# Optimization experiments

Hardware: AMD Instinct MI355X
Metric: run time of the kernel (lower is better)

The kernel has to match this reference:

```python
import jax, jax.numpy as jnp
import numpy as np

N_EMBED = 1024
N_HEAD = 16
EPS = 1.1920929e-07  # torch.finfo(float32).eps, nn.RMSNorm default eps=None


def rmsnorm(x, w):
    var = jnp.mean(x * x, axis=-1, keepdims=True)
    return x * jax.lax.rsqrt(var + EPS) * w


def setup_inputs() -> dict:
    key = jax.random.key(0)
    ks = jax.random.split(key, 12)
    d = N_EMBED
    s = lambda fan_in: 1.0 / np.sqrt(fan_in)
    inp = {
        "x": jax.random.normal(ks[0], (2, 2048, d), jnp.float32),
        "w_attn": jax.random.uniform(ks[1], (d, 3 * d), jnp.float32, -s(d), s(d)),
        "b_attn": jax.random.uniform(ks[2], (3 * d,), jnp.float32, -s(d), s(d)),
        "w_proj": jax.random.uniform(ks[3], (d, d), jnp.float32, -s(d), s(d)),
        "b_proj": jax.random.uniform(ks[4], (d,), jnp.float32, -s(d), s(d)),
        "w_fc1": jax.random.uniform(ks[5], (d, 4 * d), jnp.float32, -s(d), s(d)),
        "b_fc1": jax.random.uniform(ks[6], (4 * d,), jnp.float32, -s(d), s(d)),
        "w_fc2": jax.random.uniform(ks[7], (4 * d, d), jnp.float32, -s(4 * d), s(4 * d)),
        "b_fc2": jax.random.uniform(ks[8], (d,), jnp.float32, -s(4 * d), s(4 * d)),
        "g_norm1": jnp.ones((d,), jnp.float32),
        "g_norm2": jnp.ones((d,), jnp.float32),
    }
    return inp


def reference(x, w_attn, b_attn, w_proj, b_proj, w_fc1, b_fc1, w_fc2, b_fc2, g_norm1, g_norm2):
    B, T, d = x.shape
    H = N_HEAD
    hd = d // H

    # --- attention branch ---
    h = rmsnorm(x, g_norm1)
    qkv = h @ w_attn + b_attn  # [B,T,3d]
    q, k, v = jnp.split(qkv, 3, axis=-1)
    q = q.reshape(B, T, H, hd).transpose(0, 2, 1, 3)  # [B,H,T,hd]
    k = k.reshape(B, T, H, hd).transpose(0, 2, 1, 3)
    v = v.reshape(B, T, H, hd).transpose(0, 2, 1, 3)
    qk = jnp.einsum('bhqd,bhkd->bhqk', q, k)  # NOTE: no logit scaling (as in source)
    mask = jnp.tril(jnp.ones((T, T), bool))
    qk = jnp.where(mask, qk, -jnp.inf)
    # source scales softmax OUTPUT by n_embed**-0.5 (faithful quirk)
    attn = jax.nn.softmax(qk, axis=-1) * (d ** -0.5)
    o = jnp.einsum('bhqk,bhkd->bhqd', attn, v)
    o = o.transpose(0, 2, 1, 3).reshape(B, T, d)
    x = x + (o @ w_proj + b_proj)

    # --- MLP branch ---
    h = rmsnorm(x, g_norm2)
    h = jax.nn.gelu(h @ w_fc1 + b_fc1, approximate=False)
    x = x + (h @ w_fc2 + b_fc2)
    return x
```

## Files before the change

### kernel.cpp

```cpp
#include <hip/hip_runtime.h>
#include <hip/hip_bf16.h>


typedef __hip_bfloat16 bf16;
typedef __attribute__((ext_vector_type(8))) short short8;
typedef __attribute__((ext_vector_type(4))) float floatx4;

__device__ __forceinline__ float bits2f(unsigned short u) {
  union { unsigned int i; float f; } c; c.i = ((unsigned int)u) << 16; return c.f;
}
__device__ __forceinline__ unsigned short f2bits(float f) {
  bf16 b = __float2bfloat16(f);
  union { bf16 b; unsigned short u; } c; c.b = b; return c.u;
}

__device__ __forceinline__ void gld_lds16(const unsigned short* g, unsigned short* l) {
  __builtin_amdgcn_global_load_lds(
      (const __attribute__((address_space(1))) void*)g,
      (__attribute__((address_space(3))) void*)l, 16, 0, 0);
}

__global__ __launch_bounds__(256) void rmsnorm_r15(const float* __restrict__ x,
                                                   const float* __restrict__ g,
                                                   unsigned short* __restrict__ out)
{
  const int row = blockIdx.x, tid = threadIdx.x;
  const size_t rb = (size_t)row * 1024;
  float4 xv = *(const float4*)(x + rb + tid * 4);
  float v[4] = {xv.x, xv.y, xv.z, xv.w};
  float s = v[0]*v[0] + v[1]*v[1] + v[2]*v[2] + v[3]*v[3];
  #pragma unroll
  for (int off = 32; off > 0; off >>= 1) s += __shfl_down(s, off, 64);
  __shared__ float part[4];
  if ((tid & 63) == 0) part[tid >> 6] = s;
  __syncthreads();
  const float tot = part[0] + part[1] + part[2] + part[3];
  const float sc = rsqrtf(tot * (1.0f / 1024.0f) + 1.1920929e-07f);
  float4 gv = *(const float4*)(g + tid * 4);
  ushort4 o4 = { f2bits(v[0] * sc * gv.x), f2bits(v[1] * sc * gv.y),
                 f2bits(v[2] * sc * gv.z), f2bits(v[3] * sc * gv.w) };
  *(ushort4*)(out + rb + tid * 4) = o4;
}

__global__ __launch_bounds__(256) void wprep_r15(const float* __restrict__ in,
                                                 unsigned short* __restrict__ out,
                                                 int K, int N)
{
  __shared__ unsigned short tile[32][33];
  const int tid = threadIdx.x;
  const int k0 = blockIdx.y * 32, n0 = blockIdx.x * 32;
  const int tr = tid >> 3, tc4 = (tid & 7) * 4;
  float4 v = *(const float4*)(in + (size_t)(k0 + tr) * N + n0 + tc4);
  tile[tr][tc4 + 0] = f2bits(v.x);
  tile[tr][tc4 + 1] = f2bits(v.y);
  tile[tr][tc4 + 2] = f2bits(v.z);
  tile[tr][tc4 + 3] = f2bits(v.w);
  __syncthreads();
  ushort4 o = { tile[tc4 + 0][tr], tile[tc4 + 1][tr],
                tile[tc4 + 2][tr], tile[tc4 + 3][tr] };
  *(ushort4*)(out + (size_t)(n0 + tr) * K + k0 + tc4) = o;
}

template<int EPI>
__global__ __launch_bounds__(256) void gemm128_r15(
    const unsigned short* __restrict__ A,
    const unsigned short* __restrict__ BT,
    const float* __restrict__ bias,
    const float* __restrict__ resid,
    void* __restrict__ Cout,
    int M, int N, int K, int Klen)
{
  __shared__ __align__(16) unsigned short As[2][128 * 32];
  __shared__ __align__(16) unsigned short Bs[2][128 * 32];
  const int tid = threadIdx.x;
  const int lane = tid & 63;
  const int wv = tid >> 6;
  const int m0 = blockIdx.y * 128, n0 = blockIdx.x * 128;
  const int wm = (wv >> 1) * 64, wn = (wv & 1) * 64;
  const int kbase = blockIdx.z * Klen;

  const int s0 = tid, s1 = tid + 256;
  const int r0 = s0 >> 2, kq0 = (s0 & 3) ^ ((r0 >> 1) & 3);
  const int r1 = s1 >> 2, kq1 = (s1 & 3) ^ ((r1 >> 1) & 3);
  const unsigned short* Ab = A  + (size_t)m0 * K;
  const unsigned short* Bb = BT + (size_t)n0 * K;
  const size_t ga0 = (size_t)r0 * K + kq0 * 8 + kbase;
  const size_t ga1 = (size_t)r1 * K + kq1 * 8 + kbase;

  floatx4 acc[4][4];
  #pragma unroll
  for (int i = 0; i < 4; ++i)
    #pragma unroll
    for (int j = 0; j < 4; ++j)
      acc[i][j] = (floatx4){0.f, 0.f, 0.f, 0.f};

  int aoff[4], boff[4];
  #pragma unroll
  for (int i = 0; i < 4; ++i) {
    int ra = wm + i * 16 + (lane & 15);
    aoff[i] = (ra * 4 + ((lane >> 4) ^ ((ra >> 1) & 3))) * 8;
    int rb = wn + i * 16 + (lane & 15);
    boff[i] = (rb * 4 + ((lane >> 4) ^ ((rb >> 1) & 3))) * 8;
  }

  gld_lds16(Ab + ga0, As[0] + s0 * 8);
  gld_lds16(Ab + ga1, As[0] + s1 * 8);
  gld_lds16(Bb + ga0, Bs[0] + s0 * 8);
  gld_lds16(Bb + ga1, Bs[0] + s1 * 8);
  __syncthreads();

  const int nsteps = Klen >> 5;
  for (int t = 0; t < nsteps; ++t) {
    const int cur = t & 1;
    if (t + 1 < nsteps) {
      const size_t ko = (size_t)(t + 1) * 32;
      gld_lds16(Ab + ga0 + ko, As[cur ^ 1] + s0 * 8);
      gld_lds16(Ab + ga1 + ko, As[cur ^ 1] + s1 * 8);
      gld_lds16(Bb + ga0 + ko, Bs[cur ^ 1] + s0 * 8);
      gld_lds16(Bb + ga1 + ko, Bs[cur ^ 1] + s1 * 8);
    }

    short8 af[4], bfr[4];
    #pragma unroll
    for (int i = 0; i < 4; ++i) {
      af[i]  = *(const short8*)(As[cur] + aoff[i]);
      bfr[i] = *(const short8*)(Bs[cur] + boff[i]);
    }
    #pragma unroll
    for (int i = 0; i < 4; ++i)
      #pragma unroll
      for (int j = 0; j < 4; ++j)
        acc[i][j] = __builtin_amdgcn_mfma_f32_16x16x32_bf16(af[i], bfr[j], acc[i][j], 0, 0, 0);

    __syncthreads();
  }

  float* Cp32 = (float*)Cout;
  if constexpr (EPI == 4) Cp32 += (size_t)blockIdx.z * ((size_t)M * N);

  #pragma unroll
  for (int i = 0; i < 4; ++i) {
    #pragma unroll
    for (int j = 0; j < 4; ++j) {
      const int rbase = m0 + wm + i * 16 + (lane >> 4) * 4;
      const int c = n0 + wn + j * 16 + (lane & 15);
      float bia = 0.0f;
      if constexpr (EPI != 4) bia = bias[c];
      #pragma unroll
      for (int r = 0; r < 4; ++r) {
        float v = acc[i][j][r] + bia;
        const size_t idx = (size_t)(rbase + r) * N + c;
        if constexpr (EPI == 0) {
          ((unsigned short*)Cout)[idx] = f2bits(v);
        } else if constexpr (EPI == 1) {
          ((float*)Cout)[idx] = v + resid[idx];
        } else if constexpr (EPI == 2) {
          v = 0.5f * v * (1.0f + erff(v * 0.70710678118654752f));
          ((unsigned short*)Cout)[idx] = f2bits(v);
        } else if constexpr (EPI == 3) {
          ((float*)Cout)[idx] = v + resid[idx];
        } else {
          Cp32[idx] = v;
        }
      }
    }
  }
}

template<int EPI>
__global__ __launch_bounds__(512) void gemm256_r15(
    const unsigned short* __restrict__ A,
    const unsigned short* __restrict__ BT,
    const float* __restrict__ bias,
    void* __restrict__ Cout,
    int M, int N, int K)
{
  __shared__ __align__(16) unsigned short As[4][256 * 32];
  __shared__ __align__(16) unsigned short Bs[4][256 * 32];
  const int tid = threadIdx.x;
  const int lane = tid & 63, wv = tid >> 6;
  const int quad = lane >> 4, l15 = lane & 15;
  const int m0 = blockIdx.y * 256, n0 = blockIdx.x * 256;
  const int wm = (wv >> 2) * 128, wn = (wv & 3) * 64;

  const int s0 = tid, s1 = tid + 512;
  const int r0 = s0 >> 2, kq0 = (s0 & 3) ^ ((r0 >> 1) & 3);
  const int r1 = s1 >> 2, kq1 = (s1 & 3) ^ ((r1 >> 1) & 3);
  const unsigned short* Ab = A  + (size_t)m0 * K;
  const unsigned short* Bb = BT + (size_t)n0 * K;
  const size_t ga0 = (size_t)r0 * K + kq0 * 8;
  const size_t ga1 = (size_t)r1 * K + kq1 * 8;

  floatx4 acc[8][4];
  #pragma unroll
  for (int i = 0; i < 8; ++i)
    #pragma unroll
    for (int j = 0; j < 4; ++j)
      acc[i][j] = (floatx4){0.f, 0.f, 0.f, 0.f};

  int aoff[8], boff[4];
  #pragma unroll
  for (int i = 0; i < 8; ++i) {
    int ra = wm + i * 16 + l15;
    aoff[i] = (ra * 4 + (quad ^ ((ra >> 1) & 3))) * 8;
  }
  #pragma unroll
  for (int j = 0; j < 4; ++j) {
    int rb = wn + j * 16 + l15;
    boff[j] = (rb * 4 + (quad ^ ((rb >> 1) & 3))) * 8;
  }

  #define STG_R15(t) { const size_t ko = (size_t)(t) * 32; const int bb = (t) & 3; \
    gld_lds16(Ab + ga0 + ko, As[bb] + s0 * 8); \
    gld_lds16(Ab + ga1 + ko, As[bb] + s1 * 8); \
    gld_lds16(Bb + ga0 + ko, Bs[bb] + s0 * 8); \
    gld_lds16(Bb + ga1 + ko, Bs[bb] + s1 * 8); }

  STG_R15(0);
  STG_R15(1);

  const int nsteps = K >> 5;
  for (int t = 0; t < nsteps; ++t) {
    const int cur = t & 3;
    if (t + 2 < nsteps) {
      STG_R15(t + 2);
      asm volatile("s_waitcnt vmcnt(8)" ::: "memory");
    } else if (t + 1 < nsteps) {
      asm volatile("s_waitcnt vmcnt(4)" ::: "memory");
    } else {
      asm volatile("s_waitcnt vmcnt(0)" ::: "memory");
    }
    __builtin_amdgcn_s_barrier();
    asm volatile("" ::: "memory");

    short8 bfr[4];
    #pragma unroll
    for (int j = 0; j < 4; ++j)
      bfr[j] = *(const short8*)(Bs[cur] + boff[j]);
    #pragma unroll
    for (int ih = 0; ih < 2; ++ih) {
      short8 af[4];
      #pragma unroll
      for (int k = 0; k < 4; ++k)
        af[k] = *(const short8*)(As[cur] + aoff[ih * 4 + k]);
      #pragma unroll
      for (int k = 0; k < 4; ++k)
        #pragma unroll
        for (int j = 0; j < 4; ++j)
          acc[ih * 4 + k][j] = __builtin_amdgcn_mfma_f32_16x16x32_bf16(af[k], bfr[j], acc[ih * 4 + k][j], 0, 0, 0);
    }
  }
  #undef STG_R15

  #pragma unroll
  for (int i = 0; i < 8; ++i) {
    #pragma unroll
    for (int j = 0; j < 4; ++j) {
      const int rbase = m0 + wm + i * 16 + quad * 4;
      const int c = n0 + wn + j * 16 + l15;
      const float bia = bias[c];
      #pragma unroll
      for (int r = 0; r < 4; ++r) {
        float v = acc[i][j][r] + bia;
        const size_t idx = (size_t)(rbase + r) * N + c;
        if constexpr (EPI == 2) {
          v = 0.5f * v * (1.0f + erff(v * 0.70710678118654752f));
        }
        ((unsigned short*)Cout)[idx] = f2bits(v);
      }
    }
  }
}

__global__ __launch_bounds__(256) void red2_r15(const float* __restrict__ P,
                                                const float* __restrict__ resid,
                                                const float* __restrict__ bias,
                                                float* __restrict__ out)
{
  const size_t i = ((size_t)blockIdx.x * 256 + threadIdx.x) * 4;
  const int col = (int)(i & 1023);
  float4 p0 = *(const float4*)(P + i);
  float4 p1 = *(const float4*)(P + ((size_t)4096 * 1024) + i);
  float4 xr = *(const float4*)(resid + i);
  float4 b  = *(const float4*)(bias + col);
  float4 o  = { p0.x + p1.x + xr.x + b.x, p0.y + p1.y + xr.y + b.y,
                p0.z + p1.z + xr.z + b.z, p0.w + p1.w + xr.w + b.w };
  *(float4*)(out + i) = o;
}

__global__ __launch_bounds__(512) void attn_r15(const unsigned short* __restrict__ qkv,
                                                unsigned short* __restrict__ o)
{
  __shared__ __align__(16) unsigned short Qs[128 * 64];
  __shared__ __align__(16) unsigned short Ks[2][64 * 64];
  __shared__ __align__(16) unsigned short VT[2][64 * 72];
  __shared__ __align__(16) unsigned short Ps[128 * 72];
  __shared__ __align__(16) float stat_s[128];

  const int tid = threadIdx.x, lane = tid & 63, wv = tid >> 6;
  const int quad = lane >> 4, l15 = lane & 15;
  const int qt0 = blockIdx.x, bh = blockIdx.y;
  const int b = bh >> 4, h = bh & 15;
  const size_t base = (size_t)b * 2048 * 3072;
  const int qcol = h * 64, kcol = 1024 + h * 64, vcol = 2048 + h * 64;

  const int sr = tid >> 3, scp = tid & 7, sc = scp ^ (sr & 7);
  const unsigned short* kgp = qkv + base + (size_t)sr * 3072 + kcol + sc * 8;
  const int vp = tid & 31, vdc = tid >> 5;
  const unsigned short* vgp = qkv + base + (size_t)(2 * vp) * 3072 + vcol + vdc * 4;

  for (int pass = 0; pass < 2; ++pass) {
    const int qt = pass ? qt0 : 15 - qt0;
    const int q0 = qt * 128;
    const int nkt = 2 * qt + 2;

    __syncthreads();

    #pragma unroll
    for (int p = 0; p < 2; ++p) {
      int s = tid + 512 * p;
      int r = s >> 3, cp = s & 7, c = cp ^ (r & 7);
      gld_lds16(qkv + base + (size_t)(q0 + r) * 3072 + qcol + c * 8, Qs + s * 8);
    }
    gld_lds16(kgp, Ks[0] + tid * 8);
    {
      uint2 u0 = *(const uint2*)vgp;
      uint2 u1 = *(const uint2*)(vgp + 3072);
      unsigned short* dst = VT[0] + (size_t)(vdc * 4) * 72 + 2 * vp;
      *(unsigned int*)(dst + 0 * 72) = (u0.x & 0xffffu) | (u1.x << 16);
      *(unsigned int*)(dst + 1 * 72) = (u0.x >> 16)     | (u1.x & 0xffff0000u);
      *(unsigned int*)(dst + 2 * 72) = (u0.y & 0xffffu) | (u1.y << 16);
      *(unsigned int*)(dst + 3 * 72) = (u0.y >> 16)     | (u1.y & 0xffff0000u);
    }
    __syncthreads();

    short8 qa[2];
    #pragma unroll
    for (int ks = 0; ks < 2; ++ks) {
      int ra = wv * 16 + l15;
      int cp = (ks * 4 + quad) ^ (ra & 7);
      qa[ks] = *(const short8*)(Qs + (ra * 8 + cp) * 8);
    }

    floatx4 oacc[4];
    #pragma unroll
    for (int dt = 0; dt < 4; ++dt) oacc[dt] = (floatx4){0.f, 0.f, 0.f, 0.f};
    float m_i[4], l_i[4];
    #pragma unroll
    for (int r = 0; r < 4; ++r) { m_i[r] = -3.0e38f; l_i[r] = 0.0f; }

    for (int kt = 0; kt < nkt; ++kt) {
      const int cur = kt & 1;
      const bool pf = (kt + 1 < nkt);
      uint2 u0, u1;
      if (pf) {
        const size_t koff = (size_t)(kt + 1) * 64 * 3072;
        gld_lds16(kgp + koff, Ks[cur ^ 1] + tid * 8);
        u0 = *(const uint2*)(vgp + koff);
        u1 = *(const uint2*)(vgp + koff + 3072);
      }

      short8 kb[4][2];
      #pragma unroll
      for (int j = 0; j < 4; ++j)
        #pragma unroll
        for (int ks = 0; ks < 2; ++ks) {
          int rb = j * 16 + l15;
          int cp = (ks * 4 + quad) ^ (rb & 7);
          kb[j][ks] = *(const short8*)(Ks[cur] + (rb * 8 + cp) * 8);
        }
      floatx4 s_[4];
      #pragma unroll
      for (int j = 0; j < 4; ++j) s_[j] = (floatx4){0.f, 0.f, 0.f, 0.f};
      #pragma unroll
      for (int j = 0; j < 4; ++j)
        #pragma unroll
        for (int ks = 0; ks < 2; ++ks)
          s_[j] = __builtin_amdgcn_mfma_f32_16x16x32_bf16(qa[ks], kb[j][ks], s_[j], 0, 0, 0);

      const int k0 = kt * 64;
      const int rowmin = q0 + wv * 16;
      const int rowb = rowmin + quad * 4;
      if (k0 + 63 > rowmin) {
        #pragma unroll
        for (int j = 0; j < 4; ++j) {
          const int col = k0 + j * 16 + l15;
          #pragma unroll
          for (int r = 0; r < 4; ++r)
            if (col > rowb + r) s_[j][r] = -3.0e38f;
        }
      }
      float fm[4], al[4], rs[4];
      #pragma unroll
      for (int r = 0; r < 4; ++r)
        fm[r] = fmaxf(fmaxf(s_[0][r], s_[1][r]), fmaxf(s_[2][r], s_[3][r]));
      #pragma unroll
      for (int msk = 1; msk < 16; msk <<= 1)
        #pragma unroll
        for (int r = 0; r < 4; ++r)
          fm[r] = fmaxf(fm[r], __shfl_xor(fm[r], msk, 64));
      #pragma unroll
      for (int r = 0; r < 4; ++r) {
        const float mn = fmaxf(m_i[r], fm[r]);
        al[r] = __expf(m_i[r] - mn);
        m_i[r] = mn;
      }
      #pragma unroll
      for (int j = 0; j < 4; ++j)
        #pragma unroll
        for (int r = 0; r < 4; ++r)
          s_[j][r] = __expf(s_[j][r] - m_i[r]);
      #pragma unroll
      for (int r = 0; r < 4; ++r)
        rs[r] = (s_[0][r] + s_[1][r]) + (s_[2][r] + s_[3][r]);
      #pragma unroll
      for (int msk = 1; msk < 16; msk <<= 1)
        #pragma unroll
        for (int r = 0; r < 4; ++r)
          rs[r] += __shfl_xor(rs[r], msk, 64);
      #pragma unroll
      for (int r = 0; r < 4; ++r)
        l_i[r] = l_i[r] * al[r] + rs[r];
      if (l15 == 0) {
        float4 a4 = { al[0], al[1], al[2], al[3] };
        *(float4*)(stat_s + wv * 16 + quad * 4) = a4;
      }
      #pragma unroll
      for (int j = 0; j < 4; ++j)
        #pragma unroll
        for (int r = 0; r < 4; ++r)
          Ps[(size_t)(wv * 16 + quad * 4 + r) * 72 + j * 16 + l15] = f2bits(s_[j][r]);

      const float alq = stat_s[wv * 16 + l15];
      #pragma unroll
      for (int dt = 0; dt < 4; ++dt)
        #pragma unroll
        for (int r = 0; r < 4; ++r)
          oacc[dt][r] *= alq;

      short8 va[4][2], pb[2];
      #pragma unroll
      for (int dt = 0; dt < 4; ++dt)
        #pragma unroll
        for (int ks = 0; ks < 2; ++ks)
          va[dt][ks] = *(const short8*)(VT[cur] + (size_t)(dt * 16 + l15) * 72 + ks * 32 + quad * 8);
      #pragma unroll
      for (int ks = 0; ks < 2; ++ks)
        pb[ks] = *(const short8*)(Ps + (size_t)(wv * 16 + l15) * 72 + ks * 32 + quad * 8);
      #pragma unroll
      for (int dt = 0; dt < 4; ++dt)
        #pragma unroll
        for (int ks = 0; ks < 2; ++ks)
          oacc[dt] = __builtin_amdgcn_mfma_f32_16x16x32_bf16(va[dt][ks], pb[ks], oacc[dt], 0, 0, 0);

      if (pf) {
        unsigned short* dst = VT[cur ^ 1] + (size_t)(vdc * 4) * 72 + 2 * vp;
        *(unsigned int*)(dst + 0 * 72) = (u0.x & 0xffffu) | (u1.x << 16);
        *(unsigned int*)(dst + 1 * 72) = (u0.x >> 16)     | (u1.x & 0xffff0000u);
        *(unsigned int*)(dst + 2 * 72) = (u0.y & 0xffffu) | (u1.y << 16);
        *(unsigned int*)(dst + 3 * 72) = (u0.y >> 16)     | (u1.y & 0xffff0000u);
      }
      __syncthreads();
    }

    if (l15 == 0) {
      float4 l4 = { l_i[0], l_i[1], l_i[2], l_i[3] };
      *(float4*)(stat_s + wv * 16 + quad * 4) = l4;
    }
    const float linv = 0.03125f / stat_s[wv * 16 + l15];
    const size_t row = (size_t)b * 2048 + q0 + wv * 16 + l15;
    #pragma unroll
    for (int dt = 0; dt < 4; ++dt) {
      const int col = h * 64 + dt * 16 + quad * 4;
      ushort4 o4 = { f2bits(oacc[dt][0] * linv), f2bits(oacc[dt][1] * linv),
                     f2bits(oacc[dt][2] * linv), f2bits(oacc[dt][3] * linv) };
      *(ushort4*)(o + row * 1024 + col) = o4;
    }
  }
}

extern "C" void kernel_launch(void* const* d_in, const int* in_sizes, int n_in,
                              void* d_out, int out_size, void* d_ws, size_t ws_size,
                              hipStream_t stream)
{
  (void)in_sizes; (void)n_in; (void)out_size; (void)ws_size;
  const float* x      = (const float*)d_in[0];
  const float* w_attn = (const float*)d_in[1];
  const float* b_attn = (const float*)d_in[2];
  const float* w_proj = (const float*)d_in[3];
  const float* b_proj = (const float*)d_in[4];
  const float* w_fc1  = (const float*)d_in[5];
  const float* b_fc1  = (const float*)d_in[6];
  const float* w_fc2  = (const float*)d_in[7];
  const float* b_fc2  = (const float*)d_in[8];
  const float* g1     = (const float*)d_in[9];
  const float* g2     = (const float*)d_in[10];
  float* out = (float*)d_out;

  char* ws = (char*)d_ws;
  unsigned short* h   = (unsigned short*)(ws);
  unsigned short* qkv = (unsigned short*)(ws + ((size_t)8  << 20));
  unsigned short* ov  = (unsigned short*)(ws);
  float*          x1  = (float*)         (ws + ((size_t)32 << 20));
  unsigned short* h2  = (unsigned short*)(ws + ((size_t)8  << 20));
  unsigned short* h3  = (unsigned short*)(ws + ((size_t)48 << 20));
  unsigned short* WT  = (unsigned short*)(ws + ((size_t)80 << 20));
  float*          P   = (float*)(ws);

  const int M = 4096;

  rmsnorm_r15<<<M, 256, 0, stream>>>(x, g1, h);
  wprep_r15<<<dim3(3072 / 32, 1024 / 32), 256, 0, stream>>>(w_attn, WT, 1024, 3072);
  gemm256_r15<0><<<dim3(3072 / 256, M / 256), 512, 0, stream>>>(h, WT, b_attn, qkv, M, 3072, 1024);
  attn_r15<<<dim3(8, 32), 512, 0, stream>>>(qkv, ov);
  wprep_r15<<<dim3(1024 / 32, 1024 / 32), 256, 0, stream>>>(w_proj, WT, 1024, 1024);
  gemm128_r15<1><<<dim3(1024 / 128, M / 128), 256, 0, stream>>>(ov, WT, b_proj, x, x1, M, 1024, 1024, 1024);
  rmsnorm_r15<<<M, 256, 0, stream>>>(x1, g2, h2);
  wprep_r15<<<dim3(4096 / 32, 1024 / 32), 256, 0, stream>>>(w_fc1, WT, 1024, 4096);
  gemm256_r15<2><<<dim3(4096 / 256, M / 256), 512, 0, stream>>>(h2, WT, b_fc1, h3, M, 4096, 1024);
  wprep_r15<<<dim3(1024 / 32, 4096 / 32), 256, 0, stream>>>(w_fc2, WT, 4096, 1024);
  gemm128_r15<4><<<dim3(1024 / 128, M / 128, 2), 256, 0, stream>>>(h3, WT, nullptr, nullptr, P, M, 1024, 4096, 2048);
  red2_r15<<<4096, 256, 0, stream>>>(P, x1, b_fc2, out);
}
```

Baseline: 379.4 us.

## Deepen attention K/V prefetch to two tiles ahead with triple-buffered K

The attention kernel's key/value loop now prefetches two tiles ahead instead of one. K is triple-buffered in LDS, and V values are ping-ponged through two register sets via a manually unrolled-by-two loop. Full __syncthreads are replaced with explicit vmcnt/lgkmcnt waits plus s_barrier, to hide global load latency behind the MFMA and softmax work. The cost is extra LDS (one more K tile) and extra registers, which may reduce occupancy. Hand-tuned waitcnt values risk correctness if the instruction ordering changes.

```diff
diff --git a/kernel.cpp b/kernel.cpp
--- a/kernel.cpp
+++ b/kernel.cpp
@@ -20,7 +20,7 @@
       (__attribute__((address_space(3))) void*)l, 16, 0, 0);
 }
 
-__global__ __launch_bounds__(256) void rmsnorm_r15(const float* __restrict__ x,
+__global__ __launch_bounds__(256) void rmsnorm_r17(const float* __restrict__ x,
                                                    const float* __restrict__ g,
                                                    unsigned short* __restrict__ out)
 {
@@ -42,7 +42,7 @@
   *(ushort4*)(out + rb + tid * 4) = o4;
 }
 
-__global__ __launch_bounds__(256) void wprep_r15(const float* __restrict__ in,
+__global__ __launch_bounds__(256) void wprep_r17(const float* __restrict__ in,
                                                  unsigned short* __restrict__ out,
                                                  int K, int N)
 {
@@ -62,7 +62,7 @@
 }
 
 template<int EPI>
-__global__ __launch_bounds__(256) void gemm128_r15(
+__global__ __launch_bounds__(256) void gemm128_r17(
     const unsigned short* __restrict__ A,
     const unsigned short* __restrict__ BT,
     const float* __restrict__ bias,
@@ -168,7 +168,7 @@
 }
 
 template<int EPI>
-__global__ __launch_bounds__(512) void gemm256_r15(
+__global__ __launch_bounds__(512) void gemm256_r17(
     const unsigned short* __restrict__ A,
     const unsigned short* __restrict__ BT,
     const float* __restrict__ bias,
@@ -210,20 +210,20 @@
     boff[j] = (rb * 4 + (quad ^ ((rb >> 1) & 3))) * 8;
   }
 
-  #define STG_R15(t) { const size_t ko = (size_t)(t) * 32; const int bb = (t) & 3; \
+  #define STG_R17(t) { const size_t ko = (size_t)(t) * 32; const int bb = (t) & 3; \
     gld_lds16(Ab + ga0 + ko, As[bb] + s0 * 8); \
     gld_lds16(Ab + ga1 + ko, As[bb] + s1 * 8); \
     gld_lds16(Bb + ga0 + ko, Bs[bb] + s0 * 8); \
     gld_lds16(Bb + ga1 + ko, Bs[bb] + s1 * 8); }
 
-  STG_R15(0);
-  STG_R15(1);
+  STG_R17(0);
+  STG_R17(1);
 
   const int nsteps = K >> 5;
   for (int t = 0; t < nsteps; ++t) {
     const int cur = t & 3;
     if (t + 2 < nsteps) {
-      STG_R15(t + 2);
+      STG_R17(t + 2);
       asm volatile("s_waitcnt vmcnt(8)" ::: "memory");
     } else if (t + 1 < nsteps) {
       asm volatile("s_waitcnt vmcnt(4)" ::: "memory");
@@ -250,7 +250,7 @@
           acc[ih * 4 + k][j] = __builtin_amdgcn_mfma_f32_16x16x32_bf16(af[k], bfr[j], acc[ih * 4 + k][j], 0, 0, 0);
     }
   }
-  #undef STG_R15
+  #undef STG_R17
 
   #pragma unroll
   for (int i = 0; i < 8; ++i) {
@@ -272,7 +272,7 @@
   }
 }
 
-__global__ __launch_bounds__(256) void red2_r15(const float* __restrict__ P,
+__global__ __launch_bounds__(256) void red2_r17(const float* __restrict__ P,
                                                 const float* __restrict__ resid,
                                                 const float* __restrict__ bias,
                                                 float* __restrict__ out)
@@ -288,11 +288,11 @@
   *(float4*)(out + i) = o;
 }
 
-__global__ __launch_bounds__(512) void attn_r15(const unsigned short* __restrict__ qkv,
+__global__ __launch_bounds__(512) void attn_r17(const unsigned short* __restrict__ qkv,
                                                 unsigned short* __restrict__ o)
 {
   __shared__ __align__(16) unsigned short Qs[128 * 64];
-  __shared__ __align__(16) unsigned short Ks[2][64 * 64];
+  __shared__ __align__(16) unsigned short Ks[3][64 * 64];
   __shared__ __align__(16) unsigned short VT[2][64 * 72];
   __shared__ __align__(16) unsigned short Ps[128 * 72];
   __shared__ __align__(16) float stat_s[128];
@@ -308,6 +308,8 @@
   const unsigned short* kgp = qkv + base + (size_t)sr * 3072 + kcol + sc * 8;
   const int vp = tid & 31, vdc = tid >> 5;
   const unsigned short* vgp = qkv + base + (size_t)(2 * vp) * 3072 + vcol + vdc * 4;
+  unsigned short* KsB = &Ks[0][0];
+  const int t8 = tid * 8;
 
   for (int pass = 0; pass < 2; ++pass) {
     const int qt = pass ? qt0 : 15 - qt0;
@@ -322,17 +324,25 @@
       int r = s >> 3, cp = s & 7, c = cp ^ (r & 7);
       gld_lds16(qkv + base + (size_t)(q0 + r) * 3072 + qcol + c * 8, Qs + s * 8);
     }
-    gld_lds16(kgp, Ks[0] + tid * 8);
+    gld_lds16(kgp, KsB + t8);
+    uint2 vA0, vA1, vB0, vB1;
+    if (nkt > 1) gld_lds16(kgp + (size_t)64 * 3072, KsB + 4096 + t8);
+    vA0 = *(const uint2*)vgp;
+    vA1 = *(const uint2*)(vgp + 3072);
+    if (nkt > 1) {
+      vB0 = *(const uint2*)(vgp + (size_t)64 * 3072);
+      vB1 = *(const uint2*)(vgp + (size_t)64 * 3072 + 3072);
+    }
+    asm volatile("s_waitcnt vmcnt(2)" ::: "memory");
     {
-      uint2 u0 = *(const uint2*)vgp;
-      uint2 u1 = *(const uint2*)(vgp + 3072);
       unsigned short* dst = VT[0] + (size_t)(vdc * 4) * 72 + 2 * vp;
-      *(unsigned int*)(dst + 0 * 72) = (u0.x & 0xffffu) | (u1.x << 16);
-      *(unsigned int*)(dst + 1 * 72) = (u0.x >> 16)     | (u1.x & 0xffff0000u);
-      *(unsigned int*)(dst + 2 * 72) = (u0.y & 0xffffu) | (u1.y << 16);
-      *(unsigned int*)(dst + 3 * 72) = (u0.y >> 16)     | (u1.y & 0xffff0000u);
-    }
-    __syncthreads();
+      *(unsigned int*)(dst + 0 * 72) = (vA0.x & 0xffffu) | (vA1.x << 16);
+      *(unsigned int*)(dst + 1 * 72) = (vA0.x >> 16)     | (vA1.x & 0xffff0000u);
+      *(unsigned int*)(dst + 2 * 72) = (vA0.y & 0xffffu) | (vA1.y << 16);
+      *(unsigned int*)(dst + 3 * 72) = (vA0.y >> 16)     | (vA1.y & 0xffff0000u);
+    }
+    asm volatile("s_waitcnt lgkmcnt(0)" ::: "memory");
+    __builtin_amdgcn_s_barrier();
 
     short8 qa[2];
     #pragma unroll
@@ -349,119 +359,126 @@
     #pragma unroll
     for (int r = 0; r < 4; ++r) { m_i[r] = -3.0e38f; l_i[r] = 0.0f; }
 
-    for (int kt = 0; kt < nkt; ++kt) {
-      const int cur = kt & 1;
-      const bool pf = (kt + 1 < nkt);
-      uint2 u0, u1;
-      if (pf) {
-        const size_t koff = (size_t)(kt + 1) * 64 * 3072;
-        gld_lds16(kgp + koff, Ks[cur ^ 1] + tid * 8);
-        u0 = *(const uint2*)(vgp + koff);
-        u1 = *(const uint2*)(vgp + koff + 3072);
-      }
-
-      short8 kb[4][2];
-      #pragma unroll
-      for (int j = 0; j < 4; ++j)
-        #pragma unroll
-        for (int ks = 0; ks < 2; ++ks) {
-          int rb = j * 16 + l15;
-          int cp = (ks * 4 + quad) ^ (rb & 7);
-          kb[j][ks] = *(const short8*)(Ks[cur] + (rb * 8 + cp) * 8);
-        }
-      floatx4 s_[4];
-      #pragma unroll
-      for (int j = 0; j < 4; ++j) s_[j] = (floatx4){0.f, 0.f, 0.f, 0.f};
-      #pragma unroll
-      for (int j = 0; j < 4; ++j)
-        #pragma unroll
-        for (int ks = 0; ks < 2; ++ks)
-          s_[j] = __builtin_amdgcn_mfma_f32_16x16x32_bf16(qa[ks], kb[j][ks], s_[j], 0, 0, 0);
-
-      const int k0 = kt * 64;
-      const int rowmin = q0 + wv * 16;
-      const int rowb = rowmin + quad * 4;
-      if (k0 + 63 > rowmin) {
-        #pragma unroll
-        for (int j = 0; j < 4; ++j) {
-          const int col = k0 + j * 16 + l15;
-          #pragma unroll
-          for (int r = 0; r < 4; ++r)
-            if (col > rowb + r) s_[j][r] = -3.0e38f;
-        }
-      }
-      float fm[4], al[4], rs[4];
-      #pragma unroll
-      for (int r = 0; r < 4; ++r)
-        fm[r] = fmaxf(fmaxf(s_[0][r], s_[1][r]), fmaxf(s_[2][r], s_[3][r]));
-      #pragma unroll
-      for (int msk = 1; msk < 16; msk <<= 1)
-        #pragma unroll
-        for (int r = 0; r < 4; ++r)
-          fm[r] = fmaxf(fm[r], __shfl_xor(fm[r], msk, 64));
-      #pragma unroll
-      for (int r = 0; r < 4; ++r) {
-        const float mn = fmaxf(m_i[r], fm[r]);
-        al[r] = __expf(m_i[r] - mn);
-        m_i[r] = mn;
-      }
-      #pragma unroll
-      for (int j = 0; j < 4; ++j)
-        #pragma unroll
-        for (int r = 0; r < 4; ++r)
-          s_[j][r] = __expf(s_[j][r] - m_i[r]);
-      #pragma unroll
-      for (int r = 0; r < 4; ++r)
-        rs[r] = (s_[0][r] + s_[1][r]) + (s_[2][r] + s_[3][r]);
-      #pragma unroll
-      for (int msk = 1; msk < 16; msk <<= 1)
-        #pragma unroll
-        for (int r = 0; r < 4; ++r)
-          rs[r] += __shfl_xor(rs[r], msk, 64);
-      #pragma unroll
-      for (int r = 0; r < 4; ++r)
-        l_i[r] = l_i[r] * al[r] + rs[r];
-      if (l15 == 0) {
-        float4 a4 = { al[0], al[1], al[2], al[3] };
-        *(float4*)(stat_s + wv * 16 + quad * 4) = a4;
-      }
-      #pragma unroll
-      for (int j = 0; j < 4; ++j)
-        #pragma unroll
-        for (int r = 0; r < 4; ++r)
-          Ps[(size_t)(wv * 16 + quad * 4 + r) * 72 + j * 16 + l15] = f2bits(s_[j][r]);
-
-      const float alq = stat_s[wv * 16 + l15];
-      #pragma unroll
-      for (int dt = 0; dt < 4; ++dt)
-        #pragma unroll
-        for (int r = 0; r < 4; ++r)
-          oacc[dt][r] *= alq;
-
-      short8 va[4][2], pb[2];
-      #pragma unroll
-      for (int dt = 0; dt < 4; ++dt)
-        #pragma unroll
-        for (int ks = 0; ks < 2; ++ks)
-          va[dt][ks] = *(const short8*)(VT[cur] + (size_t)(dt * 16 + l15) * 72 + ks * 32 + quad * 8);
-      #pragma unroll
-      for (int ks = 0; ks < 2; ++ks)
-        pb[ks] = *(const short8*)(Ps + (size_t)(wv * 16 + l15) * 72 + ks * 32 + quad * 8);
-      #pragma unroll
-      for (int dt = 0; dt < 4; ++dt)
-        #pragma unroll
-        for (int ks = 0; ks < 2; ++ks)
-          oacc[dt] = __builtin_amdgcn_mfma_f32_16x16x32_bf16(va[dt][ks], pb[ks], oacc[dt], 0, 0, 0);
-
-      if (pf) {
-        unsigned short* dst = VT[cur ^ 1] + (size_t)(vdc * 4) * 72 + 2 * vp;
-        *(unsigned int*)(dst + 0 * 72) = (u0.x & 0xffffu) | (u1.x << 16);
-        *(unsigned int*)(dst + 1 * 72) = (u0.x >> 16)     | (u1.x & 0xffff0000u);
-        *(unsigned int*)(dst + 2 * 72) = (u0.y & 0xffffu) | (u1.y << 16);
-        *(unsigned int*)(dst + 3 * 72) = (u0.y >> 16)     | (u1.y & 0xffff0000u);
-      }
-      __syncthreads();
-    }
+#define AITER_R17(KT, LV0, LV1, WV0, WV1)                                        \
+    {                                                                            \
+      const int kt_ = (KT);                                                      \
+      const bool pf2_ = (kt_ + 2 < nkt);                                         \
+      const bool pf1_ = (kt_ + 1 < nkt);                                         \
+      if (pf2_) {                                                                \
+        const size_t koff_ = (size_t)(kt_ + 2) * 64 * 3072;                      \
+        gld_lds16(kgp + koff_, KsB + ((kt_ + 2) % 3) * 4096 + t8);               \
+        LV0 = *(const uint2*)(vgp + koff_);                                      \
+        LV1 = *(const uint2*)(vgp + koff_ + 3072);                               \
+      }                                                                          \
+      const unsigned short* Kcur_ = KsB + (kt_ % 3) * 4096;                      \
+      const unsigned short* Vcur_ = VT[kt_ & 1];                                 \
+      short8 kb[4][2];                                                           \
+      _Pragma("unroll")                                                          \
+      for (int j = 0; j < 4; ++j)                                                \
+        _Pragma("unroll")                                                        \
+        for (int ks = 0; ks < 2; ++ks) {                                         \
+          int rb = j * 16 + l15;                                                 \
+          int cp = (ks * 4 + quad) ^ (rb & 7);                                   \
+          kb[j][ks] = *(const short8*)(Kcur_ + (rb * 8 + cp) * 8);               \
+        }                                                                        \
+      floatx4 s_[4];                                                             \
+      _Pragma("unroll")                                                          \
+      for (int j = 0; j < 4; ++j) s_[j] = (floatx4){0.f, 0.f, 0.f, 0.f};         \
+      _Pragma("unroll")                                                          \
+      for (int j = 0; j < 4; ++j)                                                \
+        _Pragma("unroll")                                                        \
+        for (int ks = 0; ks < 2; ++ks)                                           \
+          s_[j] = __builtin_amdgcn_mfma_f32_16x16x32_bf16(qa[ks], kb[j][ks], s_[j], 0, 0, 0); \
+      const int k0_ = kt_ * 64;                                                  \
+      const int rowmin_ = q0 + wv * 16;                                          \
+      const int rowb_ = rowmin_ + quad * 4;                                      \
+      if (k0_ + 63 > rowmin_) {                                                  \
+        _Pragma("unroll")                                                        \
+        for (int j = 0; j < 4; ++j) {                                            \
+          const int col_ = k0_ + j * 16 + l15;                                   \
+          _Pragma("unroll")                                                      \
+          for (int r = 0; r < 4; ++r)                                            \
+            if (col_ > rowb_ + r) s_[j][r] = -3.0e38f;                           \
+        }                                                                        \
+      }                                                                          \
+      float fm[4], al[4], rs[4];                                                 \
+      _Pragma("unroll")                                                          \
+      for (int r = 0; r < 4; ++r)                                                \
+        fm[r] = fmaxf(fmaxf(s_[0][r], s_[1][r]), fmaxf(s_[2][r], s_[3][r]));     \
+      _Pragma("unroll")                                                          \
+      for (int msk = 1; msk < 16; msk <<= 1)                                     \
+        _Pragma("unroll")                                                        \
+        for (int r = 0; r < 4; ++r)                                              \
+          fm[r] = fmaxf(fm[r], __shfl_xor(fm[r], msk, 64));                      \
+      _Pragma("unroll")                                                          \
+      for (int r = 0; r < 4; ++r) {                                              \
+        const float mn = fmaxf(m_i[r], fm[r]);                                   \
+        al[r] = __expf(m_i[r] - mn);                                             \
+        m_i[r] = mn;                                                             \
+      }                                                                          \
+      _Pragma("unroll")                                                          \
+      for (int j = 0; j < 4; ++j)                                                \
+        _Pragma("unroll")                                                        \
+        for (int r = 0; r < 4; ++r)                                              \
+          s_[j][r] = __expf(s_[j][r] - m_i[r]);                                  \
+      _Pragma("unroll")                                                          \
+      for (int r = 0; r < 4; ++r)                                                \
+        rs[r] = (s_[0][r] + s_[1][r]) + (s_[2][r] + s_[3][r]);                   \
+      _Pragma("unroll")                                                          \
+      for (int msk = 1; msk < 16; msk <<= 1)                                     \
+        _Pragma("unroll")                                                        \
+        for (int r = 0; r < 4; ++r)                                              \
+          rs[r] += __shfl_xor(rs[r], msk, 64);                                   \
+      _Pragma("unroll")                                                          \
+      for (int r = 0; r < 4; ++r)                                                \
+        l_i[r] = l_i[r] * al[r] + rs[r];                                         \
+      if (l15 == 0) {                                                            \
+        float4 a4 = { al[0], al[1], al[2], al[3] };                              \
+        *(float4*)(stat_s + wv * 16 + quad * 4) = a4;                            \
+      }                                                                          \
+      _Pragma("unroll")                                                          \
+      for (int j = 0; j < 4; ++j)                                                \
+        _Pragma("unroll")                                                        \
+        for (int r = 0; r < 4; ++r)                                              \
+          Ps[(size_t)(wv * 16 + quad * 4 + r) * 72 + j * 16 + l15] = f2bits(s_[j][r]); \
+      const float alq_ = stat_s[wv * 16 + l15];                                  \
+      _Pragma("unroll")                                                          \
+      for (int dt = 0; dt < 4; ++dt)                                             \
+        _Pragma("unroll")                                                        \
+        for (int r = 0; r < 4; ++r)                                              \
+          oacc[dt][r] *= alq_;                                                   \
+      short8 va[4][2], pb[2];                                                    \
+      _Pragma("unroll")                                                          \
+      for (int dt = 0; dt < 4; ++dt)                                             \
+        _Pragma("unroll")                                                        \
+        for (int ks = 0; ks < 2; ++ks)                                           \
+          va[dt][ks] = *(const short8*)(Vcur_ + (size_t)(dt * 16 + l15) * 72 + ks * 32 + quad * 8); \
+      _Pragma("unroll")                                                          \
+      for (int ks = 0; ks < 2; ++ks)                                             \
+        pb[ks] = *(const short8*)(Ps + (size_t)(wv * 16 + l15) * 72 + ks * 32 + quad * 8); \
+      _Pragma("unroll")                                                          \
+      for (int dt = 0; dt < 4; ++dt)                                             \
+        _Pragma("unroll")                                                        \
+        for (int ks = 0; ks < 2; ++ks)                                           \
+          oacc[dt] = __builtin_amdgcn_mfma_f32_16x16x32_bf16(va[dt][ks], pb[ks], oacc[dt], 0, 0, 0); \
+      if (pf1_) {                                                                \
+        if (pf2_) { asm volatile("s_waitcnt vmcnt(3)" ::: "memory"); }           \
+        else      { asm volatile("s_waitcnt vmcnt(0)" ::: "memory"); }           \
+        unsigned short* dst = VT[(kt_ + 1) & 1] + (size_t)(vdc * 4) * 72 + 2 * vp; \
+        *(unsigned int*)(dst + 0 * 72) = (WV0.x & 0xffffu) | (WV1.x << 16);      \
+        *(unsigned int*)(dst + 1 * 72) = (WV0.x >> 16)     | (WV1.x & 0xffff0000u); \
+        *(unsigned int*)(dst + 2 * 72) = (WV0.y & 0xffffu) | (WV1.y << 16);      \
+        *(unsigned int*)(dst + 3 * 72) = (WV0.y >> 16)     | (WV1.y & 0xffff0000u); \
+      }                                                                          \
+      asm volatile("s_waitcnt lgkmcnt(0)" ::: "memory");                         \
+      __builtin_amdgcn_s_barrier();                                              \
+    }
+
+    for (int t = 0; t < nkt; t += 2) {
+      AITER_R17(t,     vA0, vA1, vB0, vB1);
+      AITER_R17(t + 1, vB0, vB1, vA0, vA1);
+    }
+#undef AITER_R17
 
     if (l15 == 0) {
       float4 l4 = { l_i[0], l_i[1], l_i[2], l_i[3] };
@@ -509,16 +526,16 @@
 
   const int M = 4096;
 
-  rmsnorm_r15<<<M, 256, 0, stream>>>(x, g1, h);
-  wprep_r15<<<dim3(3072 / 32, 1024 / 32), 256, 0, stream>>>(w_attn, WT, 1024, 3072);
-  gemm256_r15<0><<<dim3(3072 / 256, M / 256), 512, 0, stream>>>(h, WT, b_attn, qkv, M, 3072, 1024);
-  attn_r15<<<dim3(8, 32), 512, 0, stream>>>(qkv, ov);
-  wprep_r15<<<dim3(1024 / 32, 1024 / 32), 256, 0, stream>>>(w_proj, WT, 1024, 1024);
-  gemm128_r15<1><<<dim3(1024 / 128, M / 128), 256, 0, stream>>>(ov, WT, b_proj, x, x1, M, 1024, 1024, 1024);
-  rmsnorm_r15<<<M, 256, 0, stream>>>(x1, g2, h2);
-  wprep_r15<<<dim3(4096 / 32, 1024 / 32), 256, 0, stream>>>(w_fc1, WT, 1024, 4096);
-  gemm256_r15<2><<<dim3(4096 / 256, M / 256), 512, 0, stream>>>(h2, WT, b_fc1, h3, M, 4096, 1024);
-  wprep_r15<<<dim3(1024 / 32, 4096 / 32), 256, 0, stream>>>(w_fc2, WT, 4096, 1024);
-  gemm128_r15<4><<<dim3(1024 / 128, M / 128, 2), 256, 0, stream>>>(h3, WT, nullptr, nullptr, P, M, 1024, 4096, 2048);
-  red2_r15<<<4096, 256, 0, stream>>>(P, x1, b_fc2, out);
-}
+  rmsnorm_r17<<<M, 256, 0, stream>>>(x, g1, h);
+  wprep_r17<<<dim3(3072 / 32, 1024 / 32), 256, 0, stream>>>(w_attn, WT, 1024, 3072);
+  gemm256_r17<0><<<dim3(3072 / 256, M / 256), 512, 0, stream>>>(h, WT, b_attn, qkv, M, 3072, 1024);
+  attn_r17<<<dim3(8, 32), 512, 0, stream>>>(qkv, ov);
+  wprep_r17<<<dim3(1024 / 32, 1024 / 32), 256, 0, stream>>>(w_proj, WT, 1024, 1024);
+  gemm128_r17<1><<<dim3(1024 / 128, M / 128), 256, 0, stream>>>(ov, WT, b_proj, x, x1, M, 1024, 1024, 1024);
+  rmsnorm_r17<<<M, 256, 0, stream>>>(x1, g2, h2);
+  wprep_r17<<<dim3(4096 / 32, 1024 / 32), 256, 0, stream>>>(w_fc1, WT, 1024, 4096);
+  gemm256_r17<2><<<dim3(4096 / 256, M / 256), 512, 0, stream>>>(h2, WT, b_fc1, h3, M, 4096, 1024);
+  wprep_r17<<<dim3(1024 / 32, 4096 / 32), 256, 0, stream>>>(w_fc2, WT, 4096, 1024);
+  gemm128_r17<4><<<dim3(1024 / 128, M / 128, 2), 256, 0, stream>>>(h3, WT, nullptr, nullptr, P, M, 1024, 4096, 2048);
+  red2_r17<<<4096, 256, 0, stream>>>(P, x1, b_fc2, out);
+}
```

Result: slower. 389.7 us (+2.7%).
